# Performance work log

Hardware: AMD Instinct MI355X
Metric: run time of the kernel (lower is better)

The kernel has to match this reference:

```python
import jax, jax.numpy as jnp
import numpy as np
from jax import lax

N, CIN, H, W = 128, 1024, 14, 14
CF, TH = 128, 128          # cv_filter, te_hidden
HP, GT, FP, A = 256, 256, 256, 32


def setup_inputs() -> dict:
    key = jax.random.key(0)
    ks = jax.random.split(key, 12)
    s = 0.05
    return {
        "image": jax.random.normal(ks[0], (N, CIN, H, W), jnp.float32),
        "code": jax.random.normal(ks[1], (N, TH), jnp.float32),
        "conv_w": jax.random.normal(ks[2], (CF, CIN, 3, 3), jnp.float32) * 0.02,
        "conv_b": jnp.zeros((CF,), jnp.float32),
        "hp_w0": jax.random.normal(ks[3], (CF + 2 + TH, HP), jnp.float32) * s,
        "hp_b0": jnp.zeros((HP,), jnp.float32),
        "hp_w1": jax.random.normal(ks[4], (HP, 1), jnp.float32) * s,
        "hp_b1": jnp.zeros((1,), jnp.float32),
        "gt_w0": jax.random.normal(ks[5], ((CF + 2) * 2 + TH, GT), jnp.float32) * s,
        "gt_b0": jnp.zeros((GT,), jnp.float32),
        "gt_w1": jax.random.normal(ks[6], (GT, GT), jnp.float32) * s,
        "gt_b1": jnp.zeros((GT,), jnp.float32),
        "fp_w0": jax.random.normal(ks[7], (GT, FP), jnp.float32) * s,
        "fp_b0": jnp.zeros((FP,), jnp.float32),
        "fp_w1": jax.random.normal(ks[8], (FP, A), jnp.float32) * s,
        "fp_b1": jnp.zeros((A,), jnp.float32),
    }


def _sarn(image, code, conv_w, conv_b, hp_w0, hp_b0, hp_w1, hp_b1,
          gt_w0, gt_b0, gt_w1, gt_b1, fp_w0, fp_b0, fp_w1, fp_b1):
    # visual_resize: 3x3 conv, stride 1, pad 1 (NCHW)
    x = lax.conv_general_dilated(image, conv_w, (1, 1), "SAME",
                                 dimension_numbers=("NCHW", "OIHW", "NCHW"))
    x = x + conv_b[None, :, None, None]                       # [n, cf, h, w]
    n, c, h, w = x.shape
    o = h * w
    # sarn_encode: append x/y coordinate channels and question code
    xc = jnp.broadcast_to(jnp.linspace(-1.0, 1.0, h).reshape(1, 1, h, 1), (n, 1, h, w))
    yc = jnp.broadcast_to(jnp.linspace(-1.0, 1.0, w).reshape(1, 1, 1, w), (n, 1, h, w))
    coord = jnp.concatenate([x, xc, yc], axis=1)              # [n, cf+2, h, w]
    q = jnp.broadcast_to(code[:, :, None, None], (n, code.shape[1], h, w))
    qenc = jnp.concatenate([coord, q], axis=1)                # [n, cf+2+th, h, w]
    ce = coord.reshape(n, c + 2, o).transpose(0, 2, 1)        # [n, o, cf+2]
    qe = qenc.reshape(n, -1, o).transpose(0, 2, 1)            # [n, o, cf+2+th]
    # h_psi: per-object attention logit
    a = jax.nn.relu(jnp.einsum("nod,dh->noh", qe, hp_w0) + hp_b0)
    att = jnp.einsum("noh,hk->nok", a, hp_w1) + hp_b1         # [n, o, 1]
    # sarn_pair: softmax select a single soft object, pair with every object
    sel = jax.nn.softmax(att[..., 0], axis=1)                 # [n, o]
    selected = jnp.einsum("no,nod->nd", sel, ce)              # [n, cf+2]
    pairs = jnp.concatenate(
        [qe, jnp.broadcast_to(selected[:, None, :], ce.shape)], axis=2)  # [n, o, 2*(cf+2)+th]
    # g_theta MLP + sum over objects
    g = jax.nn.relu(jnp.einsum("nop,pg->nog", pairs, gt_w0) + gt_b0)
    g = jax.nn.relu(jnp.einsum("nog,gk->nok", g, gt_w1) + gt_b1)
    relations = g.sum(axis=1)                                 # [n, gt]
    # f_phi MLP -> answer logits
    f = jax.nn.relu(relations @ fp_w0 + fp_b0)
    return f @ fp_w1 + fp_b1                                  # [n, a_size]


def reference(image, code, conv_w, conv_b, hp_w0, hp_b0, hp_w1, hp_b1,
              gt_w0, gt_b0, gt_w1, gt_b1, fp_w0, fp_b0, fp_w1, fp_b1):
    return _sarn(image, code, conv_w, conv_b, hp_w0, hp_b0, hp_w1, hp_b1,
                 gt_w0, gt_b0, gt_w1, gt_b1, fp_w0, fp_b0, fp_w1, fp_b1)
```

## Files before the change

### kernel.cpp

```cpp
#include <hip/hip_runtime.h>
#include <stdint.h>

typedef unsigned short u16;
typedef __bf16 bf16x8 __attribute__((ext_vector_type(8)));
typedef float f32x4 __attribute__((ext_vector_type(4)));

__device__ __forceinline__ u16 f2b(float f) {
  union { float f; uint32_t u; } v; v.f = f;
  uint32_t r = v.u + 0x7fffu + ((v.u >> 16) & 1u);
  return (u16)(r >> 16);
}
__device__ __forceinline__ float b2f(u16 b) {
  union { float f; uint32_t u; } v; v.u = ((uint32_t)b) << 16;
  return v.f;
}
__device__ __forceinline__ void g2l16(const void* g, void* l) {
  __builtin_amdgcn_global_load_lds(
      (const __attribute__((address_space(1))) void*)g,
      (__attribute__((address_space(3))) void*)l, 16, 0, 0);
}

#define N_SAMP 128
#define OPAD   224
#define ROWS   (N_SAMP * OPAD)
#define KQ     160

#define R_HP   40960
#define R_GT0  40960
#define R_GT1  65536
#define R_BHP  32768
#define R_BGT  32768
#define R_QC   (ROWS * 8)
#define R_QP   114688
#define R_ATT  7168
#define R_REL  8192
#define R_CVA  917504
__global__ __launch_bounds__(256) void prep_all(
    const float* __restrict__ conv_w, const float* __restrict__ image,
    const float* __restrict__ hp_w0, const float* __restrict__ gt_w0,
    const float* __restrict__ gt_w1, const float* __restrict__ hp_b0,
    const float* __restrict__ gt_b0, const float* __restrict__ code,
    u16* __restrict__ W2, u16* __restrict__ imgT,
    u16* __restrict__ hp_w0t, u16* __restrict__ gt_w0t, u16* __restrict__ gt_w1t,
    float* __restrict__ biasHP, float* __restrict__ biasGT, u16* __restrict__ qeb,
    float* __restrict__ att, float* __restrict__ relations,
    float* __restrict__ convAcc) {
  __shared__ float ls[64 * 197];
  int bid = blockIdx.x;
  int t = threadIdx.x;

  if (bid < 512) {
    int p0 = bid << 8;
    const float* src = conv_w + (size_t)p0 * 9;
#pragma unroll
    for (int i = 0; i < 9; ++i) ls[t + i * 256] = src[t + i * 256];
    __syncthreads();
#pragma unroll
    for (int s = 0; s < 9; ++s)
      W2[s * 131072 + p0 + t] = f2b(ls[t * 9 + s]);
    return;
  }
  bid -= 512;

  if (bid < 2048) {
    float (*tt)[197] = (float(*)[197])ls;
    int n = bid >> 4;
    int cin0 = (bid & 15) * 64;
    const float* src = image + ((size_t)n * 1024 + cin0) * 196;
    for (int e = t; e < 64 * 196; e += 256) {
      int c = e / 196, sp = e % 196;
      tt[c][sp] = src[c * 196 + sp];
    }
    __syncthreads();
#pragma unroll
    for (int i = 0; i < 8; ++i) {
      int qid = t + i * 256;
      int spg = qid >> 3, qd = qid & 7;
      int gy = spg >> 4, gx = spg & 15;
      uint4 pk = {0u, 0u, 0u, 0u};
      if (gy >= 1 && gy <= 14 && gx >= 1 && gx <= 14) {
        int sp = (gy - 1) * 14 + (gx - 1);
        uint32_t vv[8];
#pragma unroll
        for (int j = 0; j < 8; ++j) vv[j] = f2b(tt[qd * 8 + j][sp]);
        pk.x = vv[0] | (vv[1] << 16);
        pk.y = vv[2] | (vv[3] << 16);
        pk.z = vv[4] | (vv[5] << 16);
        pk.w = vv[6] | (vv[7] << 16);
      }
      *(uint4*)(imgT + (((size_t)(n * 256 + spg)) << 10) + cin0 + qd * 8) = pk;
    }
    return;
  }
  bid -= 2048;

  int idx = bid * 256 + t;
  if (idx < R_HP) {
    int nn = idx / KQ, kk = idx % KQ;
    hp_w0t[idx] = (kk < 130) ? f2b(hp_w0[kk * 256 + nn]) : (u16)0;
    return;
  }
  idx -= R_HP;
  if (idx < R_GT0) {
    int nn = idx / KQ, kk = idx % KQ;
    gt_w0t[idx] = (kk < 130) ? f2b(gt_w0[kk * 256 + nn]) : (u16)0;
    return;
  }
  idx -= R_GT0;
  if (idx < R_GT1) {
    int nn = idx >> 8, kk = idx & 255;
    gt_w1t[idx] = f2b(gt_w1[kk * 256 + nn]);
    return;
  }
  idx -= R_GT1;
  if (idx < R_BHP) {
    int n = idx >> 8, tc = idx & 255;
    float acc = hp_b0[tc];
    for (int d = 0; d < 128; ++d) acc += code[n * 128 + d] * hp_w0[(130 + d) * 256 + tc];
    biasHP[idx] = acc;
    return;
  }
  idx -= R_BHP;
  if (idx < R_BGT) {
    int n = idx >> 8, tc = idx & 255;
    float acc = gt_b0[tc];
    for (int d = 0; d < 128; ++d) acc += code[n * 128 + d] * gt_w0[(130 + d) * 256 + tc];
    biasGT[idx] = acc;
    return;
  }
  idx -= R_BGT;
  if (idx < R_QC) {
    int row = idx >> 3, qd = idx & 7;
    int o = row % 224;
    ushort4 v = {0, 0, 0, 0};
    if (o < 196 && qd == 0) {
      int y = o / 14, x = o % 14;
      v.x = f2b(-1.f + 2.f * y / 13.f);
      v.y = f2b(-1.f + 2.f * x / 13.f);
    }
    *(ushort4*)(qeb + (size_t)row * KQ + 128 + qd * 4) = v;
    return;
  }
  idx -= R_QC;
  if (idx < R_QP) {
    int pr = idx >> 5, qd = idx & 31;
    int row = (pr / 28) * 224 + 196 + (pr % 28);
    *(ushort4*)(qeb + (size_t)row * KQ + qd * 4) = (ushort4){0, 0, 0, 0};
    return;
  }
  idx -= R_QP;
  if (idx < R_ATT) { *((float4*)att + idx) = (float4){0.f, 0.f, 0.f, 0.f}; return; }
  idx -= R_ATT;
  if (idx < R_REL) { *((float4*)relations + idx) = (float4){0.f, 0.f, 0.f, 0.f}; return; }
  idx -= R_REL;
  *((float4*)convAcc + idx) = (float4){0.f, 0.f, 0.f, 0.f};
}

__global__ __launch_bounds__(256) void conv_gemm(
    const u16* __restrict__ imgT, const u16* __restrict__ W2,
    float* __restrict__ convAcc) {
  __shared__ __align__(16) u16 lA[112 * 64];
  __shared__ __align__(16) u16 lB[128 * 64];
  int tid = threadIdx.x, lane = tid & 63, w = tid >> 6;
  int wg = blockIdx.x;
  int xcd = wg & 7, grp = wg >> 3;
  int n = ((grp / 6) << 3) | xcd;
  int r6 = grp % 6;
  int oh = r6 / 3, ks = r6 % 3;
  int oBase = oh * 112;
  size_t nBase = (size_t)n << 8;
  int rowIn = lane >> 3;
  int cA = ((lane & 7) ^ rowIn) << 3;

  int yxA[4];
  for (int ii = 0; ii < 4; ++ii) {
    int t = w + ii * 4;
    int o = oBase + t * 8 + rowIn;
    bool valid = o < 196;
    int y = o / 14, x = o - y * 14;
    yxA[ii] = valid ? (y * 16 + x) : 0;
  }

  f32x4 acc[7][2];
#pragma unroll
  for (int mt = 0; mt < 7; ++mt)
#pragma unroll
    for (int j = 0; j < 2; ++j) acc[mt][j] = (f32x4){0.f, 0.f, 0.f, 0.f};

  int l = lane & 15, q = lane >> 4;
  for (int si = 0; si < 3; ++si) {
    int s = ks * 3 + si;
    int off = (s / 3) * 16 + (s % 3);
    const u16* Ws = W2 + ((size_t)(s * 128) << 10);
    for (int cb = 0; cb < 16; ++cb) {
      int k0 = cb << 6;
      __syncthreads();
      g2l16(imgT + ((nBase + (size_t)(yxA[0] + off)) << 10) + k0 + cA, &lA[(w) * 512]);
      g2l16(imgT + ((nBase + (size_t)(yxA[1] + off)) << 10) + k0 + cA, &lA[(w + 4) * 512]);
      g2l16(imgT + ((nBase + (size_t)(yxA[2] + off)) << 10) + k0 + cA, &lA[(w + 8) * 512]);
      if (w < 2)
        g2l16(imgT + ((nBase + (size_t)(yxA[3] + off)) << 10) + k0 + cA, &lA[(w + 12) * 512]);
#pragma unroll
      for (int ii = 0; ii < 4; ++ii) {
        int t = w + ii * 4;
        g2l16(Ws + ((size_t)(t * 8 + rowIn) << 10) + k0 + cA, &lB[t * 512]);
      }
      __syncthreads();
#pragma unroll
      for (int kk = 0; kk < 2; ++kk) {
        int co = ((((kk << 2) | q) ^ (l & 7)) << 3);
        bf16x8 af[7];
#pragma unroll
        for (int mt = 0; mt < 7; ++mt)
          af[mt] = *(const bf16x8*)&lA[(mt * 16 + l) * 64 + co];
#pragma unroll
        for (int jj = 0; jj < 2; ++jj) {
          bf16x8 bb = *(const bf16x8*)&lB[(w * 32 + jj * 16 + l) * 64 + co];
#pragma unroll
          for (int mt = 0; mt < 7; ++mt)
            acc[mt][jj] = __builtin_amdgcn_mfma_f32_16x16x32_bf16(af[mt], bb, acc[mt][jj], 0, 0, 0);
        }
      }
    }
  }
#pragma unroll
  for (int mt = 0; mt < 7; ++mt) {
    int o = oBase + mt * 16 + q * 4;
#pragma unroll
    for (int r4 = 0; r4 < 4; ++r4) {
      if (o + r4 < 196) {
        float* dst = convAcc + (size_t)(n * 224 + o + r4) * 128 + w * 32 + l;
        atomicAdd(dst, acc[mt][0][r4]);
        atomicAdd(dst + 16, acc[mt][1][r4]);
      }
    }
  }
}

__global__ __launch_bounds__(256) void conv_fix(
    const float* __restrict__ convAcc, const float* __restrict__ conv_b,
    u16* __restrict__ qeb) {
  int idx = blockIdx.x * 256 + threadIdx.x;
  int row196 = idx >> 5;
  int c0 = (idx & 31) << 2;
  int n = row196 / 196, o = row196 - n * 196;
  size_t row = (size_t)(n * 224 + o);
  const float4 v = *(const float4*)(convAcc + (row << 7) + c0);
  const float4 b = *(const float4*)(conv_b + c0);
  ushort4 pk;
  pk.x = f2b(v.x + b.x); pk.y = f2b(v.y + b.y);
  pk.z = f2b(v.z + b.z); pk.w = f2b(v.w + b.w);
  *(ushort4*)(qeb + row * KQ + c0) = pk;
}

template <int MODE, int KP, int KC>
__global__ __launch_bounds__(256) void gemm_kernel(
    const u16* __restrict__ A, const u16* __restrict__ Bt,
    const float* __restrict__ bias, const float* __restrict__ vec,
    float* __restrict__ outF, u16* __restrict__ outB) {
  __shared__ __align__(16) u16 lA[2][128 * 32];
  __shared__ __align__(16) u16 lB[2][128 * 32];
  int tid = threadIdx.x, lane = tid & 63, w = tid >> 6;
  int bx = blockIdx.x, by = blockIdx.y;
  int r0 = bx * 112;
  int cBase = by * 128;
  int kb = (((lane & 3) ^ ((lane >> 3) & 3)) << 3);
  int rA0 = r0 + w * 16 + (lane >> 2);
  int rA1 = r0 + (w + 4) * 16 + (lane >> 2);
  const u16* gA0 = A + (size_t)rA0 * KP + kb;
  const u16* gA1 = A + (size_t)rA1 * KP + kb;
  int cB0 = cBase + w * 16 + (lane >> 2);
  int cB1 = cBase + (w + 4) * 16 + (lane >> 2);
  const u16* gB0 = Bt + (size_t)cB0 * KP + kb;
  const u16* gB1 = Bt + (size_t)cB1 * KP + kb;

  f32x4 acc[7][2];
#pragma unroll
  for (int mt = 0; mt < 7; ++mt)
#pragma unroll
    for (int j = 0; j < 2; ++j) acc[mt][j] = (f32x4){0.f, 0.f, 0.f, 0.f};
  int colW = w * 32;
  int l = lane & 15, q = lane >> 4;
  int co = ((q ^ ((l >> 1) & 3)) << 3);

  auto STAGE = [&](int buf, int cb) {
    g2l16(gA0 + cb * 32, &lA[buf][w * 512]);
    g2l16(gA1 + cb * 32, &lA[buf][(w + 4) * 512]);
    g2l16(gB0 + cb * 32, &lB[buf][w * 512]);
    g2l16(gB1 + cb * 32, &lB[buf][(w + 4) * 512]);
  };

  auto COMPUTE = [&](int cur) {
    bf16x8 af[7];
#pragma unroll
    for (int mt = 0; mt < 7; ++mt)
      af[mt] = *(const bf16x8*)&lA[cur][(mt * 16 + l) * 32 + co];
#pragma unroll
    for (int j = 0; j < 2; ++j) {
      bf16x8 bfr = *(const bf16x8*)&lB[cur][(colW + j * 16 + l) * 32 + co];
#pragma unroll
      for (int mt = 0; mt < 7; ++mt)
        acc[mt][j] = __builtin_amdgcn_mfma_f32_16x16x32_bf16(af[mt], bfr, acc[mt][j], 0, 0, 0);
    }
  };

  STAGE(0, 0);
#pragma unroll
  for (int it = 0; it < KC - 1; ++it) {
    STAGE((it & 1) ^ 1, it + 1);
    asm volatile("s_waitcnt vmcnt(4)" ::: "memory");
    __builtin_amdgcn_s_barrier();
    __builtin_amdgcn_sched_barrier(0);
    COMPUTE(it & 1);
    __builtin_amdgcn_s_barrier();
    __builtin_amdgcn_sched_barrier(0);
  }
  asm volatile("s_waitcnt vmcnt(0)" ::: "memory");
  __builtin_amdgcn_s_barrier();
  __builtin_amdgcn_sched_barrier(0);
  COMPUTE((KC - 1) & 1);

  int q4 = lane >> 4, c = lane & 15;
  if (MODE == 0) {
    int n = bx >> 1;
    float attp[7][4];
#pragma unroll
    for (int mt = 0; mt < 7; ++mt)
#pragma unroll
      for (int r = 0; r < 4; ++r) attp[mt][r] = 0.f;
#pragma unroll
    for (int j = 0; j < 2; ++j) {
      int col = cBase + colW + j * 16 + c;
      float b0 = bias[n * 256 + col], w1 = vec[col];
#pragma unroll
      for (int mt = 0; mt < 7; ++mt)
#pragma unroll
        for (int r = 0; r < 4; ++r) {
          float v = fmaxf(acc[mt][j][r] + b0, 0.f);
          attp[mt][r] += v * w1;
        }
    }
#pragma unroll
    for (int mt = 0; mt < 7; ++mt)
#pragma unroll
      for (int r = 0; r < 4; ++r) {
        float p = attp[mt][r];
        p += __shfl_xor(p, 1, 64);
        p += __shfl_xor(p, 2, 64);
        p += __shfl_xor(p, 4, 64);
        p += __shfl_xor(p, 8, 64);
        if (c == 0) atomicAdd(&outF[r0 + mt * 16 + q4 * 4 + r], p);
      }
  } else if (MODE == 1) {
    int n = bx >> 1;
#pragma unroll
    for (int mt = 0; mt < 7; ++mt)
#pragma unroll
      for (int j = 0; j < 2; ++j) {
        int col = cBase + colW + j * 16 + c;
        float b = bias[n * 256 + col];
#pragma unroll
        for (int r = 0; r < 4; ++r) {
          int row = r0 + mt * 16 + q4 * 4 + r;
          outB[(size_t)row * 256 + col] = f2b(fmaxf(acc[mt][j][r] + b, 0.f));
        }
      }
  } else {
    int n = bx >> 1;
    int ob = (bx & 1) * 112;
#pragma unroll
    for (int j = 0; j < 2; ++j) {
      int col = cBase + colW + j * 16 + c;
      float b = bias[col];
      float sum = 0.f;
#pragma unroll
      for (int mt = 0; mt < 7; ++mt)
#pragma unroll
        for (int r = 0; r < 4; ++r) {
          int o = ob + mt * 16 + q4 * 4 + r;
          if (o < 196) sum += fmaxf(acc[mt][j][r] + b, 0.f);
        }
      sum += __shfl_xor(sum, 16, 64);
      sum += __shfl_xor(sum, 32, 64);
      if (q4 == 0) atomicAdd(&outF[n * 256 + col], sum);
    }
  }
}

__global__ __launch_bounds__(256) void sel_kernel(
    const float* __restrict__ att, const u16* __restrict__ qeb,
    const float* __restrict__ gt_w0, const float* __restrict__ biasGT,
    float* __restrict__ bias2) {
  int n = blockIdx.x, t = threadIdx.x;
  int w = t >> 6, lane = t & 63;
  __shared__ u16 sq[196][130];
  __shared__ float sm[196];
  __shared__ float sel[130];
  __shared__ float red[8];
  const u16* base = qeb + (size_t)n * 224 * KQ;
  for (int o = w; o < 196; o += 4) {
    const u16* rowp = base + (size_t)o * KQ;
    for (int c = lane; c < 130; c += 64) sq[o][c] = rowp[c];
  }
  float a = (t < 196) ? att[n * 224 + t] : -1e30f;
  float m = a;
  for (int mask = 1; mask < 64; mask <<= 1) m = fmaxf(m, __shfl_xor(m, mask, 64));
  if (lane == 0) red[w] = m;
  __syncthreads();
  float M = fmaxf(fmaxf(red[0], red[1]), fmaxf(red[2], red[3]));
  float e = (t < 196) ? expf(a - M) : 0.f;
  float sAcc = e;
  for (int mask = 1; mask < 64; mask <<= 1) sAcc += __shfl_xor(sAcc, mask, 64);
  if (lane == 0) red[4 + w] = sAcc;
  __syncthreads();
  float S = red[4] + red[5] + red[6] + red[7];
  if (t < 196) sm[t] = e / S;
  __syncthreads();
  if (t < 130) {
    float acc = 0.f;
    for (int o = 0; o < 196; ++o) acc += sm[o] * b2f(sq[o][t]);
    sel[t] = acc;
  }
  __syncthreads();
  float acc2 = biasGT[n * 256 + t];
  for (int d = 0; d < 130; ++d) acc2 += sel[d] * gt_w0[(258 + d) * 256 + t];
  bias2[n * 256 + t] = acc2;
}

__global__ __launch_bounds__(256) void fphi(
    const float* __restrict__ relations, const float* __restrict__ fp_w0,
    const float* __restrict__ fp_b0, const float* __restrict__ fp_w1,
    const float* __restrict__ fp_b1, float* __restrict__ out) {
  int n = blockIdx.x, t = threadIdx.x;
  __shared__ float rel[256];
  __shared__ float f[256];
  rel[t] = relations[n * 256 + t];
  __syncthreads();
  float acc = fp_b0[t];
  for (int k = 0; k < 256; ++k) acc += rel[k] * fp_w0[k * 256 + t];
  f[t] = fmaxf(acc, 0.f);
  __syncthreads();
  if (t < 32) {
    float o = fp_b1[0];
    for (int k = 0; k < 256; ++k) o += f[k] * fp_w1[k * 32 + t];
    out[n * 32 + t] = o;
  }
}

extern "C" void kernel_launch(void* const* d_in, const int* in_sizes, int n_in,
                              void* d_out, int out_size, void* d_ws, size_t ws_size,
                              hipStream_t stream) {
  const float* image = (const float*)d_in[0];
  const float* code = (const float*)d_in[1];
  const float* conv_w = (const float*)d_in[2];
  const float* conv_b = (const float*)d_in[3];
  const float* hp_w0 = (const float*)d_in[4];
  const float* hp_b0 = (const float*)d_in[5];
  const float* hp_w1 = (const float*)d_in[6];
  const float* gt_w0 = (const float*)d_in[8];
  const float* gt_b0 = (const float*)d_in[9];
  const float* gt_w1 = (const float*)d_in[10];
  const float* gt_b1 = (const float*)d_in[11];
  const float* fp_w0 = (const float*)d_in[12];
  const float* fp_b0 = (const float*)d_in[13];
  const float* fp_w1 = (const float*)d_in[14];
  const float* fp_b1 = (const float*)d_in[15];
  float* out = (float*)d_out;

  char* p = (char*)d_ws;
  u16* imgT = (u16*)p;   p += (size_t)128 * 256 * 1024 * 2;
  u16* W2 = (u16*)p;     p += (size_t)9 * 128 * 1024 * 2;
  u16* qeb = (u16*)p;    p += (size_t)ROWS * KQ * 2;
  u16* hp_w0t = (u16*)p; p += (size_t)256 * KQ * 2;
  u16* gt_w0t = (u16*)p; p += (size_t)256 * KQ * 2;
  u16* gt_w1t = (u16*)p; p += (size_t)256 * 256 * 2;
  float* att = (float*)p;    p += (size_t)ROWS * 4;
  float* bias2 = (float*)p;  p += (size_t)128 * 256 * 4;
  float* biasHP = (float*)p; p += (size_t)128 * 256 * 4;
  float* biasGT = (float*)p; p += (size_t)128 * 256 * 4;
  float* convAcc = (float*)p; p += (size_t)ROWS * 128 * 4;
  float* relations = (float*)p; p += (size_t)128 * 256 * 4;
  u16* g1 = (u16*)convAcc;

  prep_all<<<8380, 256, 0, stream>>>(conv_w, image, hp_w0, gt_w0, gt_w1, hp_b0, gt_b0,
                                     code, W2, imgT, hp_w0t, gt_w0t, gt_w1t,
                                     biasHP, biasGT, qeb, att, relations, convAcc);
  conv_gemm<<<768, 256, 0, stream>>>(imgT, W2, convAcc);
  conv_fix<<<3136, 256, 0, stream>>>(convAcc, conv_b, qeb);
  gemm_kernel<0, KQ, 5><<<dim3(256, 2), 256, 0, stream>>>(qeb, hp_w0t, biasHP, hp_w1, att, nullptr);
  sel_kernel<<<128, 256, 0, stream>>>(att, qeb, gt_w0, biasGT, bias2);
  gemm_kernel<1, KQ, 5><<<dim3(256, 2), 256, 0, stream>>>(qeb, gt_w0t, bias2, nullptr, nullptr, g1);
  gemm_kernel<2, 256, 8><<<dim3(256, 2), 256, 0, stream>>>(g1, gt_w1t, gt_b1, nullptr, relations, nullptr);
  fphi<<<128, 256, 0, stream>>>(relations, fp_w0, fp_b0, fp_w1, fp_b1, out);
}
```

Before: 368.0 us.

## Fuse g_theta MLP layers and f_phi into one kernel with panel in LDS

Merges the two g_theta GEMMs into a single kernel that writes the first-layer activations to an LDS panel instead of global memory, then runs the second GEMM from LDS. The f_phi MLP is folded in through a per-sample completion counter, so the last block for each sample computes the logits. This removes the global round trip of the hidden activations and two kernel launches. In exchange each block handles all 256 columns, giving only 256 blocks with large LDS and register use, which lowers parallelism.

Measured after the change: 369.2 us. No clear change (+0.3%).

```diff
diff --git a/kernel.cpp b/kernel.cpp
--- a/kernel.cpp
+++ b/kernel.cpp
@@ -34,6 +34,7 @@
 #define R_QP   114688
 #define R_ATT  7168
 #define R_REL  8192
+#define R_CNT  32
 #define R_CVA  917504
 __global__ __launch_bounds__(256) void prep_all(
     const float* __restrict__ conv_w, const float* __restrict__ image,
@@ -44,7 +45,7 @@
     u16* __restrict__ hp_w0t, u16* __restrict__ gt_w0t, u16* __restrict__ gt_w1t,
     float* __restrict__ biasHP, float* __restrict__ biasGT, u16* __restrict__ qeb,
     float* __restrict__ att, float* __restrict__ relations,
-    float* __restrict__ convAcc) {
+    int* __restrict__ doneCnt, float* __restrict__ convAcc) {
   __shared__ float ls[64 * 197];
   int bid = blockIdx.x;
   int t = threadIdx.x;
@@ -153,7 +154,9 @@
   idx -= R_ATT;
   if (idx < R_REL) { *((float4*)relations + idx) = (float4){0.f, 0.f, 0.f, 0.f}; return; }
   idx -= R_REL;
-  *((float4*)convAcc + idx) = (float4){0.f, 0.f, 0.f, 0.f};
+  if (idx < R_CNT) { *((float4*)doneCnt + idx) = (float4){0.f, 0.f, 0.f, 0.f}; return; }
+  idx -= R_CNT;
+  if (idx < R_CVA) *((float4*)convAcc + idx) = (float4){0.f, 0.f, 0.f, 0.f};
 }
 
 __global__ __launch_bounds__(256) void conv_gemm(
@@ -321,7 +324,7 @@
   COMPUTE((KC - 1) & 1);
 
   int q4 = lane >> 4, c = lane & 15;
-  if (MODE == 0) {
+  {
     int n = bx >> 1;
     float attp[7][4];
 #pragma unroll
@@ -351,39 +354,6 @@
         p += __shfl_xor(p, 8, 64);
         if (c == 0) atomicAdd(&outF[r0 + mt * 16 + q4 * 4 + r], p);
       }
-  } else if (MODE == 1) {
-    int n = bx >> 1;
-#pragma unroll
-    for (int mt = 0; mt < 7; ++mt)
-#pragma unroll
-      for (int j = 0; j < 2; ++j) {
-        int col = cBase + colW + j * 16 + c;
-        float b = bias[n * 256 + col];
-#pragma unroll
-        for (int r = 0; r < 4; ++r) {
-          int row = r0 + mt * 16 + q4 * 4 + r;
-          outB[(size_t)row * 256 + col] = f2b(fmaxf(acc[mt][j][r] + b, 0.f));
-        }
-      }
-  } else {
-    int n = bx >> 1;
-    int ob = (bx & 1) * 112;
-#pragma unroll
-    for (int j = 0; j < 2; ++j) {
-      int col = cBase + colW + j * 16 + c;
-      float b = bias[col];
-      float sum = 0.f;
-#pragma unroll
-      for (int mt = 0; mt < 7; ++mt)
-#pragma unroll
-        for (int r = 0; r < 4; ++r) {
-          int o = ob + mt * 16 + q4 * 4 + r;
-          if (o < 196) sum += fmaxf(acc[mt][j][r] + b, 0.f);
-        }
-      sum += __shfl_xor(sum, 16, 64);
-      sum += __shfl_xor(sum, 32, 64);
-      if (q4 == 0) atomicAdd(&outF[n * 256 + col], sum);
-    }
   }
 }
 
@@ -427,23 +397,168 @@
   bias2[n * 256 + t] = acc2;
 }
 
-__global__ __launch_bounds__(256) void fphi(
-    const float* __restrict__ relations, const float* __restrict__ fp_w0,
+__global__ __launch_bounds__(256) void g_fused(
+    const u16* __restrict__ qeb, const u16* __restrict__ gt_w0t,
+    const u16* __restrict__ gt_w1t, const float* __restrict__ bias2,
+    const float* __restrict__ gt_b1, const float* __restrict__ fp_w0,
     const float* __restrict__ fp_b0, const float* __restrict__ fp_w1,
-    const float* __restrict__ fp_b1, float* __restrict__ out) {
-  int n = blockIdx.x, t = threadIdx.x;
-  __shared__ float rel[256];
-  __shared__ float f[256];
-  rel[t] = relations[n * 256 + t];
+    const float* __restrict__ fp_b1, float* __restrict__ relations,
+    int* __restrict__ doneCnt, float* __restrict__ out) {
+  __shared__ __align__(16) u16 panel[112 * 256];
+  __shared__ __align__(16) u16 lA[2][128 * 32];
+  __shared__ __align__(16) u16 lB[2][256 * 32];
+  __shared__ int flag;
+  int tid = threadIdx.x, lane = tid & 63, w = tid >> 6;
+  int bx = blockIdx.x;
+  int n = bx >> 1;
+  int r0 = bx * 112;
+  int kb = (((lane & 3) ^ ((lane >> 3) & 3)) << 3);
+  int rowIn = lane >> 2;
+  const u16* gA0 = qeb + (size_t)(r0 + w * 16 + rowIn) * KQ + kb;
+  const u16* gA1 = qeb + (size_t)(r0 + (w + 4) * 16 + rowIn) * KQ + kb;
+  int l = lane & 15, q = lane >> 4;
+  int co = ((q ^ ((l >> 1) & 3)) << 3);
+
+  f32x4 acc[7][4];
+#pragma unroll
+  for (int mt = 0; mt < 7; ++mt)
+#pragma unroll
+    for (int j = 0; j < 4; ++j) acc[mt][j] = (f32x4){0.f, 0.f, 0.f, 0.f};
+
+  auto STAGE1 = [&](int buf, int cb) {
+    g2l16(gA0 + cb * 32, &lA[buf][w * 512]);
+    g2l16(gA1 + cb * 32, &lA[buf][(w + 4) * 512]);
+#pragma unroll
+    for (int ii = 0; ii < 4; ++ii) {
+      int t = w + ii * 4;
+      g2l16(gt_w0t + (size_t)(t * 16 + rowIn) * KQ + kb + cb * 32, &lB[buf][t * 512]);
+    }
+  };
+  auto COMPUTE1 = [&](int cur) {
+    bf16x8 af[7];
+#pragma unroll
+    for (int mt = 0; mt < 7; ++mt)
+      af[mt] = *(const bf16x8*)&lA[cur][(mt * 16 + l) * 32 + co];
+#pragma unroll
+    for (int j = 0; j < 4; ++j) {
+      bf16x8 bfr = *(const bf16x8*)&lB[cur][(w * 64 + j * 16 + l) * 32 + co];
+#pragma unroll
+      for (int mt = 0; mt < 7; ++mt)
+        acc[mt][j] = __builtin_amdgcn_mfma_f32_16x16x32_bf16(af[mt], bfr, acc[mt][j], 0, 0, 0);
+    }
+  };
+
+  STAGE1(0, 0);
+#pragma unroll
+  for (int it = 0; it < 4; ++it) {
+    STAGE1((it + 1) & 1, it + 1);
+    asm volatile("s_waitcnt vmcnt(6)" ::: "memory");
+    __builtin_amdgcn_s_barrier();
+    __builtin_amdgcn_sched_barrier(0);
+    COMPUTE1(it & 1);
+    __builtin_amdgcn_s_barrier();
+    __builtin_amdgcn_sched_barrier(0);
+  }
+  asm volatile("s_waitcnt vmcnt(0)" ::: "memory");
+  __builtin_amdgcn_s_barrier();
+  __builtin_amdgcn_sched_barrier(0);
+  COMPUTE1(0);
+
+  auto STAGE2 = [&](int buf, int kb2) {
+#pragma unroll
+    for (int ii = 0; ii < 4; ++ii) {
+      int t = w + ii * 4;
+      g2l16(gt_w1t + (size_t)(t * 16 + rowIn) * 256 + kb + kb2 * 32, &lB[buf][t * 512]);
+    }
+  };
+  STAGE2(1, 0);
+
+#pragma unroll
+  for (int j = 0; j < 4; ++j) {
+    int col = w * 64 + j * 16 + l;
+    float b = bias2[n * 256 + col];
+    int chA = col >> 3, inA = col & 7;
+#pragma unroll
+    for (int mt = 0; mt < 7; ++mt)
+#pragma unroll
+      for (int r = 0; r < 4; ++r) {
+        int row = mt * 16 + q * 4 + r;
+        float v = fmaxf(acc[mt][j][r] + b, 0.f);
+        panel[row * 256 + ((chA ^ (row & 7)) << 3) + inA] = f2b(v);
+      }
+  }
   __syncthreads();
-  float acc = fp_b0[t];
-  for (int k = 0; k < 256; ++k) acc += rel[k] * fp_w0[k * 256 + t];
-  f[t] = fmaxf(acc, 0.f);
+
+  f32x4 acc2[7][4];
+#pragma unroll
+  for (int mt = 0; mt < 7; ++mt)
+#pragma unroll
+    for (int j = 0; j < 4; ++j) acc2[mt][j] = (f32x4){0.f, 0.f, 0.f, 0.f};
+
+#pragma unroll
+  for (int kb2 = 0; kb2 < 8; ++kb2) {
+    if (kb2 < 7) {
+      STAGE2(kb2 & 1, kb2 + 1);
+      asm volatile("s_waitcnt vmcnt(4)" ::: "memory");
+    } else {
+      asm volatile("s_waitcnt vmcnt(0)" ::: "memory");
+    }
+    __builtin_amdgcn_s_barrier();
+    __builtin_amdgcn_sched_barrier(0);
+    int cur = 1 - (kb2 & 1);
+    bf16x8 af[7];
+#pragma unroll
+    for (int mt = 0; mt < 7; ++mt) {
+      int row = mt * 16 + l;
+      int ch = (kb2 * 4 + q) ^ (row & 7);
+      af[mt] = *(const bf16x8*)&panel[row * 256 + (ch << 3)];
+    }
+#pragma unroll
+    for (int j = 0; j < 4; ++j) {
+      bf16x8 bfr = *(const bf16x8*)&lB[cur][(w * 64 + j * 16 + l) * 32 + co];
+#pragma unroll
+      for (int mt = 0; mt < 7; ++mt)
+        acc2[mt][j] = __builtin_amdgcn_mfma_f32_16x16x32_bf16(af[mt], bfr, acc2[mt][j], 0, 0, 0);
+    }
+    __builtin_amdgcn_s_barrier();
+    __builtin_amdgcn_sched_barrier(0);
+  }
+
+  int ob = (bx & 1) * 112;
+#pragma unroll
+  for (int j = 0; j < 4; ++j) {
+    int col = w * 64 + j * 16 + l;
+    float b = gt_b1[col];
+    float sum = 0.f;
+#pragma unroll
+    for (int mt = 0; mt < 7; ++mt)
+#pragma unroll
+      for (int r = 0; r < 4; ++r) {
+        int o = ob + mt * 16 + q * 4 + r;
+        if (o < 196) sum += fmaxf(acc2[mt][j][r] + b, 0.f);
+      }
+    sum += __shfl_xor(sum, 16, 64);
+    sum += __shfl_xor(sum, 32, 64);
+    if (q == 0) atomicAdd(&relations[n * 256 + col], sum);
+  }
+
+  __threadfence();
+  if (tid == 0) flag = atomicAdd(&doneCnt[n], 1);
   __syncthreads();
-  if (t < 32) {
-    float o = fp_b1[0];
-    for (int k = 0; k < 256; ++k) o += f[k] * fp_w1[k * 32 + t];
-    out[n * 32 + t] = o;
+  if (flag == 1) {
+    float* rel = (float*)panel;
+    float* f = rel + 256;
+    rel[tid] = atomicAdd(&relations[n * 256 + tid], 0.0f);
+    __syncthreads();
+    float acc3 = fp_b0[tid];
+    for (int k = 0; k < 256; ++k) acc3 += rel[k] * fp_w0[k * 256 + tid];
+    f[tid] = fmaxf(acc3, 0.f);
+    __syncthreads();
+    if (tid < 32) {
+      float o = fp_b1[0];
+      for (int k = 0; k < 256; ++k) o += f[k] * fp_w1[k * 32 + tid];
+      out[n * 32 + tid] = o;
+    }
   }
 }
 
@@ -480,16 +595,15 @@
   float* biasGT = (float*)p; p += (size_t)128 * 256 * 4;
   float* convAcc = (float*)p; p += (size_t)ROWS * 128 * 4;
   float* relations = (float*)p; p += (size_t)128 * 256 * 4;
-  u16* g1 = (u16*)convAcc;
-
-  prep_all<<<8380, 256, 0, stream>>>(conv_w, image, hp_w0, gt_w0, gt_w1, hp_b0, gt_b0,
+  int* doneCnt = (int*)p; p += 512;
+
+  prep_all<<<8381, 256, 0, stream>>>(conv_w, image, hp_w0, gt_w0, gt_w1, hp_b0, gt_b0,
                                      code, W2, imgT, hp_w0t, gt_w0t, gt_w1t,
-                                     biasHP, biasGT, qeb, att, relations, convAcc);
+                                     biasHP, biasGT, qeb, att, relations, doneCnt, convAcc);
   conv_gemm<<<768, 256, 0, stream>>>(imgT, W2, convAcc);
   conv_fix<<<3136, 256, 0, stream>>>(convAcc, conv_b, qeb);
   gemm_kernel<0, KQ, 5><<<dim3(256, 2), 256, 0, stream>>>(qeb, hp_w0t, biasHP, hp_w1, att, nullptr);
   sel_kernel<<<128, 256, 0, stream>>>(att, qeb, gt_w0, biasGT, bias2);
-  gemm_kernel<1, KQ, 5><<<dim3(256, 2), 256, 0, stream>>>(qeb, gt_w0t, bias2, nullptr, nullptr, g1);
-  gemm_kernel<2, 256, 8><<<dim3(256, 2), 256, 0, stream>>>(g1, gt_w1t, gt_b1, nullptr, relations, nullptr);
-  fphi<<<128, 256, 0, stream>>>(relations, fp_w0, fp_b0, fp_w1, fp_b1, out);
-}
+  g_fused<<<256, 256, 0, stream>>>(qeb, gt_w0t, gt_w1t, bias2, gt_b1,
+                                   fp_w0, fp_b0, fp_w1, fp_b1, relations, doneCnt, out);
+}
```
